# Kernel optimization log

Hardware: AMD Instinct MI355X
Metric: run time of the kernel (lower is better)

The kernel has to match this reference:

```python
import jax, jax.numpy as jnp
import numpy as np

B, N, D = 2, 2048, 768
H = 12
HD = D // H
HID = 4 * D
SCALE = HD ** -0.5
EPS = 1e-5


def layer_norm(x, g, b):
    mu = jnp.mean(x, axis=-1, keepdims=True)
    var = jnp.var(x, axis=-1, keepdims=True)
    return (x - mu) * jax.lax.rsqrt(var + EPS) * g + b


def setup_inputs() -> dict:
    key = jax.random.key(0)
    ks = jax.random.split(key, 12)
    s = 0.02
    return {
        "x": jax.random.normal(ks[0], (B, N, D), jnp.float32),
        "att_mask": jax.random.randint(ks[1], (B, N), 0, 2, jnp.int32),
        "ln1_g": jnp.ones((D,), jnp.float32),
        "ln1_b": jnp.zeros((D,), jnp.float32),
        "qkv_w": jax.random.normal(ks[2], (3 * D, D), jnp.float32) * s,
        "q_bias": jnp.zeros((D,), jnp.float32),
        "v_bias": jnp.zeros((D,), jnp.float32),
        "proj_w": jax.random.normal(ks[3], (D, D), jnp.float32) * s,
        "proj_b": jnp.zeros((D,), jnp.float32),
        "ln2_g": jnp.ones((D,), jnp.float32),
        "ln2_b": jnp.zeros((D,), jnp.float32),
        "fc1_w": jax.random.normal(ks[4], (HID, D), jnp.float32) * s,
        "fc1_b": jnp.zeros((HID,), jnp.float32),
        "fc2_w": jax.random.normal(ks[5], (D, HID), jnp.float32) * s,
        "fc2_b": jnp.zeros((D,), jnp.float32),
        "gamma_1": 0.1 * jnp.ones((D,), jnp.float32),
        "gamma_2": 0.1 * jnp.ones((D,), jnp.float32),
    }


def reference(x, att_mask, ln1_g, ln1_b, qkv_w, q_bias, v_bias, proj_w, proj_b,
              ln2_g, ln2_b, fc1_w, fc1_b, fc2_w, fc2_b, gamma_1, gamma_2):
    # --- attention branch ---
    h = layer_norm(x, ln1_g, ln1_b)
    qkv_bias = jnp.concatenate([q_bias, jnp.zeros_like(v_bias), v_bias])
    qkv = h @ qkv_w.T + qkv_bias                      # [B,N,3D]
    qkv = qkv.reshape(B, N, 3, H, HD).transpose(2, 0, 3, 1, 4)
    q, k, v = qkv[0], qkv[1], qkv[2]                  # [B,H,N,HD]
    logit = jnp.einsum('bhqd,bhkd->bhqk', q * SCALE, k)
    mask = att_mask[:, None, None, :]                 # key mask [B,1,1,N]
    logit = jnp.where(mask == 0, -jnp.inf, logit)
    attn = jax.nn.softmax(logit, axis=-1)
    o = jnp.einsum('bhqk,bhkd->bhqd', attn, v)
    o = o.transpose(0, 2, 1, 3).reshape(B, N, D)
    o = o @ proj_w.T + proj_b
    x = x + gamma_1 * o
    # --- mlp branch ---
    h2 = layer_norm(x, ln2_g, ln2_b)
    h2 = jax.nn.gelu(h2 @ fc1_w.T + fc1_b, approximate=False)
    h2 = h2 @ fc2_w.T + fc2_b
    return x + gamma_2 * h2
```

## Files before the change

### kernel.cpp

```cpp
#include <hip/hip_runtime.h>
#include <hip/hip_bf16.h>
#include <stdint.h>

typedef __bf16 bf16x8 __attribute__((ext_vector_type(8)));
typedef __bf16 bf16x2 __attribute__((ext_vector_type(2)));
typedef unsigned short u16x8 __attribute__((ext_vector_type(8)));
typedef float f32x4 __attribute__((ext_vector_type(4)));
typedef float f32x16 __attribute__((ext_vector_type(16)));
typedef uint32_t u32x4 __attribute__((ext_vector_type(4)));

#define DMODEL 768
#define NSEQ   2048
#define BATCH  2
#define NHEAD  12
#define HDIM   64
#define HIDDEN 3072
#define PROWS  (BATCH * NHEAD * NSEQ)
#define NZ     4
#define QSCALE 0.18033688011112042f
#define MCONST 16.0f
#define PMASKED 1.52587890625e-05f

__device__ __forceinline__ uint16_t f2bf(float f) {
  __bf16 h = (__bf16)f;
  return __builtin_bit_cast(uint16_t, h);
}
__device__ __forceinline__ float bf2f(uint16_t u) {
  uint32_t x = (uint32_t)u << 16;
  return __builtin_bit_cast(float, x);
}
__device__ __forceinline__ bf16x8 ldb8(const uint16_t* p) {
  return __builtin_bit_cast(bf16x8, *reinterpret_cast<const u16x8*>(p));
}
__device__ __forceinline__ float gelu_f(float x) {
  float u = x * (1.0f + 0.044715f * x * x);
  float e = fminf(u * 2.302208545f, 80.0f);
  float t = exp2f(e);
  return x * t / (t + 1.0f);
}

using as1_void = __attribute__((address_space(1))) const void;
using as3_void = __attribute__((address_space(3))) void;
__device__ __forceinline__ void gload16(const uint16_t* src, uint16_t* lds) {
  __builtin_amdgcn_global_load_lds((as1_void*)src, (as3_void*)lds, 16, 0, 0);
}
#define MEMFENCE asm volatile("" ::: "memory")

#define N_QKVW  (3 * DMODEL * DMODEL)
#define N_PROJW (DMODEL * DMODEL)
#define N_FC1W  (HIDDEN * DMODEL)
#define N_FC2W  (DMODEL * HIDDEN)
__global__ __launch_bounds__(256) void cvt4_kernel(const float* __restrict__ s0,
                                                   const float* __restrict__ s1,
                                                   const float* __restrict__ s2,
                                                   const float* __restrict__ s3,
                                                   uint16_t* __restrict__ d0,
                                                   uint16_t* __restrict__ d1,
                                                   uint16_t* __restrict__ d2,
                                                   uint16_t* __restrict__ d3) {
  int i4 = (blockIdx.x * 256 + threadIdx.x) * 4;
  const float* s;
  uint16_t* d;
  if (i4 < N_QKVW) { s = s0 + i4; d = d0 + i4; }
  else if (i4 < N_QKVW + N_PROJW) { int j = i4 - N_QKVW; s = s1 + j; d = d1 + j; }
  else if (i4 < N_QKVW + N_PROJW + N_FC1W) { int j = i4 - N_QKVW - N_PROJW; s = s2 + j; d = d2 + j; }
  else { int j = i4 - N_QKVW - N_PROJW - N_FC1W; s = s3 + j; d = d3 + j; }
  float4 v = *reinterpret_cast<const float4*>(s);
  ushort4 o;
  o.x = f2bf(v.x); o.y = f2bf(v.y); o.z = f2bf(v.z); o.w = f2bf(v.w);
  *reinterpret_cast<ushort4*>(d) = o;
}

__global__ __launch_bounds__(256) void bias_kernel(const float* __restrict__ qb,
                                                   const float* __restrict__ vb,
                                                   float* __restrict__ out) {
  int j = blockIdx.x * 256 + threadIdx.x;
  if (j < 3 * DMODEL) {
    float v = 0.f;
    if (j < DMODEL) v = qb[j];
    else if (j >= 2 * DMODEL) v = vb[j - 2 * DMODEL];
    out[j] = v;
  }
}

__global__ __launch_bounds__(256) void ln_kernel(const float* __restrict__ x,
                                                 const float* __restrict__ g,
                                                 const float* __restrict__ bt,
                                                 uint16_t* __restrict__ out) {
  const int row = blockIdx.x;
  const int t = threadIdx.x;
  const float* xr = x + (size_t)row * DMODEL;
  float v0 = xr[t], v1 = xr[t + 256], v2 = xr[t + 512];
  float s = v0 + v1 + v2;
  float q = v0 * v0 + v1 * v1 + v2 * v2;
  for (int off = 32; off >= 1; off >>= 1) {
    s += __shfl_xor(s, off);
    q += __shfl_xor(q, off);
  }
  __shared__ float ss[4], sq[4];
  int w = t >> 6;
  if ((t & 63) == 0) { ss[w] = s; sq[w] = q; }
  __syncthreads();
  s = ss[0] + ss[1] + ss[2] + ss[3];
  q = sq[0] + sq[1] + sq[2] + sq[3];
  const float mean = s * (1.0f / DMODEL);
  const float var = q * (1.0f / DMODEL) - mean * mean;
  const float rstd = rsqrtf(var + 1e-5f);
  uint16_t* orow = out + (size_t)row * DMODEL;
  orow[t]       = f2bf((v0 - mean) * rstd * g[t]       + bt[t]);
  orow[t + 256] = f2bf((v1 - mean) * rstd * g[t + 256] + bt[t + 256]);
  orow[t + 512] = f2bf((v2 - mean) * rstd * g[t + 512] + bt[t + 512]);
}

template <int MODE>
__global__ __launch_bounds__(256, 3) void gemm128(const uint16_t* __restrict__ A,
                                                  const uint16_t* __restrict__ W,
                                                  const float* __restrict__ bias,
                                                  void* __restrict__ outp,
                                                  uint16_t* __restrict__ km,
                                                  uint16_t* __restrict__ vt,
                                                  const int* __restrict__ amask,
                                                  int M, int N, int K) {
  __shared__ uint16_t As[2][128 * 32];
  __shared__ uint16_t Bs[2][128 * 32];
  const int tid = threadIdx.x;
  const int lane = tid & 63;
  const int w = tid >> 6;
  const int wr = w >> 1, wc = w & 1;
  const int row0 = blockIdx.y * 128;
  const int col0 = blockIdx.x * 128;
  const int lr = lane & 15;
  const int g = lane >> 4;

  const int o0 = w * 1024 + lane * 16;
  const int o1 = o0 + 4096;
  const int r0s = o0 >> 6, c0s = (o0 & 63) >> 1;
  const int r1s = o1 >> 6, c1s = (o1 & 63) >> 1;
  const int l0 = (w * 1024) >> 1;
  const int l1 = l0 + 2048;
  const uint16_t* Abase = A + (size_t)row0 * K;
  const uint16_t* Wbase = W + (size_t)col0 * K;

  auto stage = [&](int kt) {
    uint16_t* Ad = &As[kt & 1][0];
    uint16_t* Bd = &Bs[kt & 1][0];
    const int kk = kt * 32;
    gload16(Abase + (size_t)r0s * K + kk + c0s, Ad + l0);
    gload16(Abase + (size_t)r1s * K + kk + c1s, Ad + l1);
    gload16(Wbase + (size_t)r0s * K + kk + c0s, Bd + l0);
    gload16(Wbase + (size_t)r1s * K + kk + c1s, Bd + l1);
  };

  f32x4 acc[4][4] = {};
  const int nt = K >> 5;
  stage(0);
  for (int kt = 0; kt < nt; ++kt) {
    if (kt + 1 < nt) {
      stage(kt + 1);
      asm volatile("s_waitcnt vmcnt(4)" ::: "memory");
    } else {
      asm volatile("s_waitcnt vmcnt(0)" ::: "memory");
    }
    __builtin_amdgcn_s_barrier();
    MEMFENCE;
    const uint16_t* Ab = &As[kt & 1][0];
    const uint16_t* Bb = &Bs[kt & 1][0];
    bf16x8 a[4], b[4];
#pragma unroll
    for (int m = 0; m < 4; ++m) a[m] = ldb8(Ab + (wr * 64 + m * 16 + lr) * 32 + g * 8);
#pragma unroll
    for (int n = 0; n < 4; ++n) b[n] = ldb8(Bb + (wc * 64 + n * 16 + lr) * 32 + g * 8);
#pragma unroll
    for (int m = 0; m < 4; ++m)
#pragma unroll
      for (int n = 0; n < 4; ++n)
        acc[m][n] = __builtin_amdgcn_mfma_f32_16x16x32_bf16(a[m], b[n], acc[m][n], 0, 0, 0);
    MEMFENCE;
    __builtin_amdgcn_s_barrier();
  }

  if constexpr (MODE == 0) {
    const int sect = col0 / DMODEL;
    const int bb = row0 >> 11;
    const int* mrow = amask + bb * NSEQ;
#pragma unroll
    for (int m = 0; m < 4; ++m) {
      int row = row0 + wr * 64 + m * 16 + g * 4;
      int nn = row & 2047;
      int mk[4];
#pragma unroll
      for (int ri = 0; ri < 4; ++ri) mk[ri] = mrow[nn + ri];
#pragma unroll
      for (int n = 0; n < 4; ++n) {
        int col = col0 + wc * 64 + n * 16 + lr;
        float bv = bias[col];
        if (sect == 0) {
#pragma unroll
          for (int ri = 0; ri < 4; ++ri)
            ((uint16_t*)outp)[(size_t)(row + ri) * DMODEL + col] =
                f2bf((acc[m][n][ri] + bv) * QSCALE);
        } else if (sect == 1) {
          int kc = col - DMODEL;
#pragma unroll
          for (int ri = 0; ri < 4; ++ri)
            km[(size_t)(row + ri) * DMODEL + kc] =
                mk[ri] ? f2bf(acc[m][n][ri] + bv) : (uint16_t)0;
        } else {
          int vc = col - 2 * DMODEL;
          int hh2 = vc >> 6, dd = vc & 63;
          ushort4 sv;
          sv.x = mk[0] ? f2bf(acc[m][n][0] + bv) : (uint16_t)0;
          sv.y = mk[1] ? f2bf(acc[m][n][1] + bv) : (uint16_t)0;
          sv.z = mk[2] ? f2bf(acc[m][n][2] + bv) : (uint16_t)0;
          sv.w = mk[3] ? f2bf(acc[m][n][3] + bv) : (uint16_t)0;
          *reinterpret_cast<ushort4*>(
              vt + ((size_t)((bb * NHEAD + hh2) * 64 + dd)) * NSEQ + nn) = sv;
        }
      }
    }
  } else {
#pragma unroll
    for (int m = 0; m < 4; ++m) {
      int row = row0 + wr * 64 + m * 16 + g * 4;
#pragma unroll
      for (int n = 0; n < 4; ++n) {
        int col = col0 + wc * 64 + n * 16 + lr;
        float bv = bias[col];
#pragma unroll
        for (int ri = 0; ri < 4; ++ri) {
          float val = acc[m][n][ri] + bv;
          ((uint16_t*)outp)[(size_t)(row + ri) * N + col] = f2bf(gelu_f(val));
        }
      }
    }
  }
}

__global__ __launch_bounds__(256, 3) void gemm64(const uint16_t* __restrict__ A,
                                                 const uint16_t* __restrict__ W,
                                                 const float* __restrict__ bias,
                                                 float* __restrict__ outp,
                                                 const float* __restrict__ resid,
                                                 const float* __restrict__ gamma,
                                                 int M, int N, int K) {
  __shared__ uint16_t As[2][64 * 64];
  __shared__ uint16_t Bs[2][64 * 64];
  const int tid = threadIdx.x;
  const int lane = tid & 63;
  const int w = tid >> 6;
  const int wr = w >> 1, wc = w & 1;
  const int row0 = blockIdx.y * 64;
  const int col0 = blockIdx.x * 64;
  const int lr = lane & 15;
  const int g = lane >> 4;

  const int srow = tid >> 3;
  const int schunk = tid & 7;
  const uint16_t* Abase = A + (size_t)row0 * K;
  const uint16_t* Wbase = W + (size_t)col0 * K;

  auto stage = [&](int kt) {
    uint16_t* Ad = &As[kt & 1][0];
    uint16_t* Bd = &Bs[kt & 1][0];
    const int kk = kt * 64;
#pragma unroll
    for (int i = 0; i < 2; ++i) {
      const int row = i * 32 + srow;
      const int sc = (schunk ^ (row & 7)) * 8;
      gload16(Abase + (size_t)row * K + kk + sc, Ad + i * 2048 + w * 512);
      gload16(Wbase + (size_t)row * K + kk + sc, Bd + i * 2048 + w * 512);
    }
  };

  f32x4 acc[2][2] = {};
  const int nt = K >> 6;
  stage(0);
  for (int kt = 0; kt < nt; ++kt) {
    if (kt + 1 < nt) {
      stage(kt + 1);
      asm volatile("s_waitcnt vmcnt(4)" ::: "memory");
    } else {
      asm volatile("s_waitcnt vmcnt(0)" ::: "memory");
    }
    __builtin_amdgcn_s_barrier();
    MEMFENCE;
    const uint16_t* Ab = &As[kt & 1][0];
    const uint16_t* Bb = &Bs[kt & 1][0];
#pragma unroll
    for (int kk = 0; kk < 2; ++kk) {
      bf16x8 a[2], bf[2];
#pragma unroll
      for (int m = 0; m < 2; ++m) {
        const int row = wr * 32 + m * 16 + lr;
        a[m] = ldb8(Ab + row * 64 + (((kk * 4 + g) ^ (row & 7)) * 8));
      }
#pragma unroll
      for (int n = 0; n < 2; ++n) {
        const int row = wc * 32 + n * 16 + lr;
        bf[n] = ldb8(Bb + row * 64 + (((kk * 4 + g) ^ (row & 7)) * 8));
      }
#pragma unroll
      for (int m = 0; m < 2; ++m)
#pragma unroll
        for (int n = 0; n < 2; ++n)
          acc[m][n] = __builtin_amdgcn_mfma_f32_16x16x32_bf16(a[m], bf[n], acc[m][n], 0, 0, 0);
    }
    MEMFENCE;
    __builtin_amdgcn_s_barrier();
  }

#pragma unroll
  for (int m = 0; m < 2; ++m) {
    int row = row0 + wr * 32 + m * 16 + g * 4;
#pragma unroll
    for (int n = 0; n < 2; ++n) {
      int col = col0 + wc * 32 + n * 16 + lr;
      float bv = bias[col];
      float gv = gamma[col];
#pragma unroll
      for (int ri = 0; ri < 4; ++ri) {
        float val = acc[m][n][ri] + bv;
        size_t idx = (size_t)(row + ri) * N + col;
        outp[idx] = resid[idx] + gv * val;
      }
    }
  }
}

__global__ __launch_bounds__(512, 4) void attn_kernel(const uint16_t* __restrict__ qb_,
                                                      const uint16_t* __restrict__ km,
                                                      const uint16_t* __restrict__ vt,
                                                      const int* __restrict__ mask,
                                                      uint16_t* __restrict__ po,
                                                      float* __restrict__ pml) {
  __shared__ uint16_t Kb[2][64 * 64];
  __shared__ uint16_t Vb[2][64 * 64];
  __shared__ unsigned long long mbits[8];
  const int tid = threadIdx.x;
  const int lane = tid & 63;
  const int w = tid >> 6;
  const int bh = blockIdx.x;
  const int b = bh / NHEAD, hd = bh % NHEAD;
  const int z = blockIdx.z;
  const int kbase = z * 512;
  const int q0 = blockIdx.y * 256 + w * 32;
  const int l31 = lane & 31;
  const int hh = lane >> 5;

  const int* mb = mask + b * NSEQ;
  {
    unsigned long long bm = __ballot(mb[kbase + w * 64 + lane] != 0);
    if (lane == 0) mbits[w] = bm;
  }

  bf16x8 qa[4];
  const uint16_t* qptr = qb_ + (size_t)(b * NSEQ + q0 + l31) * DMODEL + hd * HDIM + hh * 8;
#pragma unroll
  for (int dblk = 0; dblk < 4; ++dblk) qa[dblk] = ldb8(qptr + dblk * 16);

  const uint16_t* kmb = km + (size_t)b * NSEQ * DMODEL + hd * HDIM;
  const uint16_t* vtb = vt + (size_t)bh * HDIM * NSEQ;

  __syncthreads();

  const int srow = tid >> 3;
  const int sxor = ((tid & 7) ^ (srow & 7)) * 8;
  auto stage = [&](int t) {
    const int pb = t & 1;
    const int k0 = kbase + t * 64;
    gload16(kmb + (size_t)(k0 + srow) * DMODEL + sxor, &Kb[pb][w * 512]);
    gload16(vtb + (size_t)srow * NSEQ + k0 + sxor, &Vb[pb][w * 512]);
  };

  u16x8 ones_u;
#pragma unroll
  for (int e = 0; e < 8; ++e) ones_u[e] = 0x3F80;
  const bf16x8 ones = __builtin_bit_cast(bf16x8, ones_u);

  f32x16 oacc[2] = {};
  f32x16 lacc = {};

  stage(0);
  for (int t = 0; t < 8; ++t) {
    if (t + 1 < 8) {
      stage(t + 1);
      asm volatile("s_waitcnt vmcnt(2)" ::: "memory");
    } else {
      asm volatile("s_waitcnt vmcnt(0)" ::: "memory");
    }
    __builtin_amdgcn_s_barrier();
    MEMFENCE;
    const uint16_t* Kbp = &Kb[t & 1][0];
    const uint16_t* Vbp = &Vb[t & 1][0];

    f32x16 st[2];
    __builtin_amdgcn_s_setprio(1);
#pragma unroll
    for (int kblk = 0; kblk < 2; ++kblk) {
      f32x16 acc = {};
      const uint16_t* kr = Kbp + (kblk * 32 + l31) * 64;
#pragma unroll
      for (int dblk = 0; dblk < 4; ++dblk) {
        bf16x8 kf = ldb8(kr + ((dblk * 2 + hh) ^ (l31 & 7)) * 8);
        acc = __builtin_amdgcn_mfma_f32_32x32x16_bf16(kf, qa[dblk], acc, 0, 0, 0);
      }
      st[kblk] = acc;
    }
    __builtin_amdgcn_s_setprio(0);

    uint32_t pk[2][8];
#pragma unroll
    for (int kblk = 0; kblk < 2; ++kblk)
#pragma unroll
      for (int wn = 0; wn < 8; ++wn) {
        float e0 = exp2f(st[kblk][2 * wn] - MCONST);
        float e1 = exp2f(st[kblk][2 * wn + 1] - MCONST);
        bf16x2 pr = {(__bf16)e0, (__bf16)e1};
        pk[kblk][wn] = __builtin_bit_cast(uint32_t, pr);
      }

    bf16x8 af[4];
#pragma unroll
    for (int kb16 = 0; kb16 < 4; ++kb16) {
      const int kblk = kb16 >> 1;
      const int a4 = (kb16 & 1) * 4;
      uint32_t ow0 = hh ? pk[kblk][a4 + 2] : pk[kblk][a4 + 0];
      uint32_t ow1 = hh ? pk[kblk][a4 + 3] : pk[kblk][a4 + 1];
      uint32_t gv0 = hh ? pk[kblk][a4 + 0] : pk[kblk][a4 + 2];
      uint32_t gv1 = hh ? pk[kblk][a4 + 1] : pk[kblk][a4 + 3];
      uint32_t sw0 = (uint32_t)__shfl_xor((int)gv0, 32);
      uint32_t sw1 = (uint32_t)__shfl_xor((int)gv1, 32);
      u32x4 afu;
      afu[0] = hh ? sw0 : ow0;
      afu[1] = hh ? sw1 : ow1;
      afu[2] = hh ? ow0 : sw0;
      afu[3] = hh ? ow1 : sw1;
      af[kb16] = __builtin_bit_cast(bf16x8, afu);
    }

    __builtin_amdgcn_s_setprio(1);
#pragma unroll
    for (int dblk = 0; dblk < 2; ++dblk) {
      const uint16_t* vr = Vbp + (dblk * 32 + l31) * 64;
#pragma unroll
      for (int kb16 = 0; kb16 < 4; ++kb16) {
        bf16x8 vf = ldb8(vr + ((kb16 * 2 + hh) ^ (l31 & 7)) * 8);
        oacc[dblk] = __builtin_amdgcn_mfma_f32_32x32x16_bf16(af[kb16], vf, oacc[dblk], 0, 0, 0);
      }
    }
#pragma unroll
    for (int kb16 = 0; kb16 < 4; ++kb16)
      lacc = __builtin_amdgcn_mfma_f32_32x32x16_bf16(af[kb16], ones, lacc, 0, 0, 0);
    __builtin_amdgcn_s_setprio(0);
    MEMFENCE;
    __builtin_amdgcn_s_barrier();
  }

  int cnt = 0;
#pragma unroll
  for (int it = 0; it < 8; ++it) cnt += 64 - __popcll(mbits[it]);
  const float cntf = (float)cnt * PMASKED;

  uint16_t* ob = po + ((size_t)z * PROWS + (size_t)bh * NSEQ + q0) * 64;
#pragma unroll
  for (int r = 0; r < 16; ++r) {
    const int qrow = (r & 3) + 8 * (r >> 2) + 4 * hh;
#pragma unroll
    for (int dblk = 0; dblk < 2; ++dblk)
      ob[(size_t)qrow * 64 + dblk * 32 + l31] = f2bf(oacc[dblk][r]);
  }
  if (l31 == 0) {
#pragma unroll
    for (int r = 0; r < 16; ++r) {
      const int qrow = (r & 3) + 8 * (r >> 2) + 4 * hh;
      pml[(size_t)z * PROWS + (size_t)bh * NSEQ + q0 + qrow] = lacc[r] - cntf;
    }
  }
}

__global__ __launch_bounds__(256) void merge_kernel(const uint16_t* __restrict__ po,
                                                    const float* __restrict__ pml,
                                                    uint16_t* __restrict__ o) {
  int gid = blockIdx.x * 256 + threadIdx.x;
  int row = gid >> 3;
  int c0 = (gid & 7) * 8;
  float L = 0.f;
#pragma unroll
  for (int zz = 0; zz < NZ; ++zz) L += pml[(size_t)zz * PROWS + row];
  float inv = L > 0.f ? 1.f / L : 0.f;
  float sum[8] = {};
#pragma unroll
  for (int zz = 0; zz < NZ; ++zz) {
    u16x8 a = *reinterpret_cast<const u16x8*>(po + ((size_t)zz * PROWS + row) * 64 + c0);
#pragma unroll
    for (int e = 0; e < 8; ++e) sum[e] += bf2f(a[e]);
  }
  int bh = row >> 11, q = row & 2047;
  int bb = bh / NHEAD, hh = bh % NHEAD;
  uint16_t* op = o + ((size_t)(bb * NSEQ + q) * DMODEL + hh * HDIM + c0);
  u16x8 outv;
#pragma unroll
  for (int e = 0; e < 8; ++e) outv[e] = f2bf(sum[e] * inv);
  *reinterpret_cast<u16x8*>(op) = outv;
}

extern "C" void kernel_launch(void* const* d_in, const int* in_sizes, int n_in,
                              void* d_out, int out_size, void* d_ws, size_t ws_size,
                              hipStream_t stream) {
  const float* x      = (const float*)d_in[0];
  const int*   amask  = (const int*)d_in[1];
  const float* ln1_g  = (const float*)d_in[2];
  const float* ln1_b  = (const float*)d_in[3];
  const float* qkv_w  = (const float*)d_in[4];
  const float* q_bias = (const float*)d_in[5];
  const float* v_bias = (const float*)d_in[6];
  const float* proj_w = (const float*)d_in[7];
  const float* proj_b = (const float*)d_in[8];
  const float* ln2_g  = (const float*)d_in[9];
  const float* ln2_b  = (const float*)d_in[10];
  const float* fc1_w  = (const float*)d_in[11];
  const float* fc1_b  = (const float*)d_in[12];
  const float* fc2_w  = (const float*)d_in[13];
  const float* fc2_b  = (const float*)d_in[14];
  const float* g1     = (const float*)d_in[15];
  const float* g2     = (const float*)d_in[16];

  char* ws = (char*)d_ws;
  uint16_t* qkvw_bf  = (uint16_t*)(ws + 0);
  uint16_t* projw_bf = (uint16_t*)(ws + 3538944);
  uint16_t* fc1w_bf  = (uint16_t*)(ws + 4718592);
  uint16_t* fc2w_bf  = (uint16_t*)(ws + 9437184);
  float*    qkvbias  = (float*)(ws + 14155776);
  uint16_t* h_bf     = (uint16_t*)(ws + 14164992);
  uint16_t* q_bf     = (uint16_t*)(ws + 20456448);
  uint16_t* km       = (uint16_t*)(ws + 26747904);
  uint16_t* vt_bf    = (uint16_t*)(ws + 33039360);
  uint16_t* po       = (uint16_t*)(ws + 39330816);
  float*    pml      = (float*)(ws + 64496640);
  uint16_t* o_bf     = q_bf;
  float*    x1_f     = (float*)(ws + 26747904);
  uint16_t* fc1_bf   = (uint16_t*)(ws + 39330816);
  uint16_t* h2_bf    = h_bf;

  const int M = BATCH * NSEQ;

  cvt4_kernel<<<(N_QKVW + N_PROJW + N_FC1W + N_FC2W) / 1024, 256, 0, stream>>>(
      qkv_w, proj_w, fc1_w, fc2_w, qkvw_bf, projw_bf, fc1w_bf, fc2w_bf);
  bias_kernel<<<(3 * DMODEL + 255) / 256, 256, 0, stream>>>(q_bias, v_bias, qkvbias);

  ln_kernel<<<M, 256, 0, stream>>>(x, ln1_g, ln1_b, h_bf);
  gemm128<0><<<dim3((3 * DMODEL) / 128, M / 128), 256, 0, stream>>>(
      h_bf, qkvw_bf, qkvbias, q_bf, km, vt_bf, amask, M, 3 * DMODEL, DMODEL);
  attn_kernel<<<dim3(BATCH * NHEAD, NSEQ / 256, NZ), 512, 0, stream>>>(
      q_bf, km, vt_bf, amask, po, pml);
  merge_kernel<<<(PROWS * 8) / 256, 256, 0, stream>>>(po, pml, o_bf);
  gemm64<<<dim3(DMODEL / 64, M / 64), 256, 0, stream>>>(
      o_bf, projw_bf, proj_b, x1_f, x, g1, M, DMODEL, DMODEL);
  ln_kernel<<<M, 256, 0, stream>>>(x1_f, ln2_g, ln2_b, h2_bf);
  gemm128<2><<<dim3(HIDDEN / 128, M / 128), 256, 0, stream>>>(
      h2_bf, fc1w_bf, fc1_b, fc1_bf, nullptr, nullptr, nullptr, M, HIDDEN, DMODEL);
  gemm64<<<dim3(DMODEL / 64, M / 64), 256, 0, stream>>>(
      fc1_bf, fc2w_bf, fc2_b, (float*)d_out, x1_f, g2, M, DMODEL, HIDDEN);
}
```

Before: 190.2 us.

## Deepen attention K/V prefetch to four buffers and swizzle GEMM blocks across XCDs

The attention kernel moves from a double-buffered to a four-slot K/V ring with three tiles in flight. The next tile's loads are issued after the barrier, so the trailing per-iteration barrier can be dropped, which is meant to hide global load latency better. Both GEMM kernels remap block indices so consecutive tiles land on the same XCD, aiming for better L2 reuse. The attention kernel's LDS use doubles to 64KB per block, which may reduce occupancy at 512 threads with the requested 4 blocks per CU.

```diff
diff --git a/kernel.cpp b/kernel.cpp
--- a/kernel.cpp
+++ b/kernel.cpp
@@ -37,6 +37,14 @@
   float e = fminf(u * 2.302208545f, 80.0f);
   float t = exp2f(e);
   return x * t / (t + 1.0f);
+}
+__device__ __forceinline__ void xcd_swz(int& bx, int& by) {
+  const int gx = gridDim.x;
+  const int nwg = gx * gridDim.y;
+  const int orig = blockIdx.y * gx + blockIdx.x;
+  const int wg = (orig & 7) * (nwg >> 3) + (orig >> 3);
+  bx = wg % gx;
+  by = wg / gx;
 }
 
 using as1_void = __attribute__((address_space(1))) const void;
@@ -127,8 +135,10 @@
   const int lane = tid & 63;
   const int w = tid >> 6;
   const int wr = w >> 1, wc = w & 1;
-  const int row0 = blockIdx.y * 128;
-  const int col0 = blockIdx.x * 128;
+  int bx, by;
+  xcd_swz(bx, by);
+  const int row0 = by * 128;
+  const int col0 = bx * 128;
   const int lr = lane & 15;
   const int g = lane >> 4;
 
@@ -249,8 +259,10 @@
   const int lane = tid & 63;
   const int w = tid >> 6;
   const int wr = w >> 1, wc = w & 1;
-  const int row0 = blockIdx.y * 64;
-  const int col0 = blockIdx.x * 64;
+  int bx, by;
+  xcd_swz(bx, by);
+  const int row0 = by * 64;
+  const int col0 = bx * 64;
   const int lr = lane & 15;
   const int g = lane >> 4;
 
@@ -333,8 +345,8 @@
                                                       const int* __restrict__ mask,
                                                       uint16_t* __restrict__ po,
                                                       float* __restrict__ pml) {
-  __shared__ uint16_t Kb[2][64 * 64];
-  __shared__ uint16_t Vb[2][64 * 64];
+  __shared__ uint16_t Kb[4][64 * 64];
+  __shared__ uint16_t Vb[4][64 * 64];
   __shared__ unsigned long long mbits[8];
   const int tid = threadIdx.x;
   const int lane = tid & 63;
@@ -366,7 +378,7 @@
   const int srow = tid >> 3;
   const int sxor = ((tid & 7) ^ (srow & 7)) * 8;
   auto stage = [&](int t) {
-    const int pb = t & 1;
+    const int pb = t & 3;
     const int k0 = kbase + t * 64;
     gload16(kmb + (size_t)(k0 + srow) * DMODEL + sxor, &Kb[pb][w * 512]);
     gload16(vtb + (size_t)srow * NSEQ + k0 + sxor, &Vb[pb][w * 512]);
@@ -381,17 +393,22 @@
   f32x16 lacc = {};
 
   stage(0);
+  stage(1);
+  stage(2);
+#pragma unroll
   for (int t = 0; t < 8; ++t) {
-    if (t + 1 < 8) {
-      stage(t + 1);
+    if (t < 6) {
+      asm volatile("s_waitcnt vmcnt(4)" ::: "memory");
+    } else if (t == 6) {
       asm volatile("s_waitcnt vmcnt(2)" ::: "memory");
     } else {
       asm volatile("s_waitcnt vmcnt(0)" ::: "memory");
     }
     __builtin_amdgcn_s_barrier();
     MEMFENCE;
-    const uint16_t* Kbp = &Kb[t & 1][0];
-    const uint16_t* Vbp = &Vb[t & 1][0];
+    if (t + 3 < 8) stage(t + 3);
+    const uint16_t* Kbp = &Kb[t & 3][0];
+    const uint16_t* Vbp = &Vb[t & 3][0];
 
     f32x16 st[2];
     __builtin_amdgcn_s_setprio(1);
@@ -453,7 +470,6 @@
       lacc = __builtin_amdgcn_mfma_f32_32x32x16_bf16(af[kb16], ones, lacc, 0, 0, 0);
     __builtin_amdgcn_s_setprio(0);
     MEMFENCE;
-    __builtin_amdgcn_s_barrier();
   }
 
   int cnt = 0;
```

Measured after the change: 180.6 us. 1.05x faster.
